# Performance work log

Hardware: AMD Instinct MI355X
Metric: run time of the kernel (lower is better)

Reference implementation:

```python
import jax, jax.numpy as jnp
import numpy as np

N_USER = 100000
N_ITEM = 100000
D = 64
N_INTER = 1600000
N_LAYERS = 3
REG_WEIGHT = 1e-4
BPR_GAMMA = 1e-10  # RecBole BPRLoss gamma
B, S = 4096, 6     # 1 positive + (S-2)=4 negatives per row


def setup_inputs() -> dict:
    rng = np.random.default_rng(0)
    u = rng.integers(0, N_USER, N_INTER)
    it = rng.integers(0, N_ITEM, N_INTER)
    pairs = np.unique(np.stack([u, it], 1), axis=0)  # dok dict dedupes
    u, it = pairs[:, 0], pairs[:, 1]
    N = N_USER + N_ITEM
    row = np.concatenate([u, it + N_USER])
    col = np.concatenate([it + N_USER, u])
    deg = np.bincount(row, minlength=N).astype(np.float64) + 1e-7
    dinv = np.power(deg, -0.5)
    val = (dinv[row] * dinv[col]).astype(np.float32)  # D^-1/2 A D^-1/2

    key = jax.random.key(0)
    k1, k2, k3, k4 = jax.random.split(key, 4)
    user_w = jax.random.normal(k1, (N_USER, D), jnp.float32) * 0.01
    item_w = jax.random.normal(k2, (N_ITEM, D), jnp.float32) * 0.01
    # padding_idx=0 -> row 0 zeroed
    user_w = user_w.at[0].set(0.0)
    item_w = item_w.at[0].set(0.0)

    xu = jax.random.randint(k3, (B, S, 1), 0, N_USER, jnp.int32)
    xi = jax.random.randint(k4, (B, S, 1), 0, N_ITEM, jnp.int32)
    pad = jnp.zeros((B, S, 2), jnp.int32)  # last 2 cols unused by forward
    x = jnp.concatenate([xu, xi, pad], axis=-1)

    return {
        "x": x,
        "user_w": user_w,
        "item_w": item_w,
        "adj_row": jnp.asarray(row, jnp.int32),
        "adj_col": jnp.asarray(col, jnp.int32),
        "adj_val": jnp.asarray(val, jnp.float32),
    }


def _propagate(user_w, item_w, adj_row, adj_col, adj_val):
    N = user_w.shape[0] + item_w.shape[0]
    h = jnp.concatenate([user_w, item_w], axis=0)  # [N, D]
    out = h  # layer-0 term of the stacked sum
    for i in range(N_LAYERS):
        # SpMM: h <- A_hat @ h  via gather + segment_sum over edges
        h = jax.ops.segment_sum(adj_val[:, None] * h[adj_col], adj_row, num_segments=N)
        # F.normalize(h, dim=-1)
        h = h / jnp.maximum(jnp.linalg.norm(h, axis=-1, keepdims=True), 1e-12)
        # result list appends h/(i+1) AND h each layer
        out = out + h / (i + 1) + h
    return out


def reference(x, user_w, item_w, adj_row, adj_col, adj_val):
    emb = _propagate(user_w, item_w, adj_row, adj_col, adj_val)
    user_emb, item_emb = emb[:N_USER], emb[N_USER:]

    p = x[:, 0, :]                       # [B, 4]
    n = x[:, 1:-1, :].reshape(-1, 4)     # [B*(S-2), 4]
    p_score = jnp.sum(user_emb[p[:, 0]] * item_emb[p[:, 1]], axis=-1)     # [B]
    n_score = jnp.sum(user_emb[n[:, 0]] * item_emb[n[:, 1]], axis=-1)
    n_score = n_score.reshape(x.shape[0], -1).sum(axis=-1)                # [B]

    bpr_loss = -jnp.mean(jnp.log(BPR_GAMMA + jax.nn.sigmoid(p_score - n_score)))
    # RecBole EmbLoss(norm=2): (||U||_F + ||I||_F) / n_item
    emb_loss = (jnp.linalg.norm(user_w) + jnp.linalg.norm(item_w)) / item_w.shape[0]
    return bpr_loss + REG_WEIGHT * emb_loss
```

## Files before the change

### kernel.cpp

```cpp
#include <hip/hip_runtime.h>
#include <hip/hip_fp16.h>

#define N_USER_C 100000
#define N_ITEM_C 100000
#define D_C 64
#define NN_C (N_USER_C + N_ITEM_C)
#define ND_C (NN_C * D_C)

#define BSHIFT 8
#define NBUCKET ((N_ITEM_C + 255) >> BSHIFT)
#define PB_CHUNK 8192

#define CONV_NBLK 1024
#define SCORE_NBLK 1024

typedef unsigned u32x4 __attribute__((ext_vector_type(4)));

union HP8 { u32x4 u; __half2 h[4]; };


__global__ __launch_bounds__(256) void edge_scan_kernel(
        const int* __restrict__ arow, const int* __restrict__ acol,
        int* __restrict__ bcnt, int* __restrict__ row_ptr_u, int ne) {
    __shared__ int s[NBUCKET];
    for (int i = threadIdx.x; i < NBUCKET; i += 256) s[i] = 0;
    __syncthreads();
    int stride = gridDim.x * blockDim.x;
    for (int e = blockIdx.x * blockDim.x + threadIdx.x; e <= ne; e += stride) {
        if (e < ne) atomicAdd(&s[(acol[e] - N_USER_C) >> BSHIFT], 1);
        int prev = (e == 0) ? -1 : arow[e - 1];
        int cur = (e == ne) ? N_USER_C : arow[e];
        for (int r = prev + 1; r <= cur; ++r) row_ptr_u[r] = e;
    }
    __syncthreads();
    for (int i = threadIdx.x; i < NBUCKET; i += 256)
        if (s[i]) atomicAdd(&bcnt[i], s[i]);
}

__global__ void bucket_scan_kernel(const int* __restrict__ bcnt, int* __restrict__ boff,
                                   int* __restrict__ row_ptr_i, int ne) {
    __shared__ int s[512];
    int t = threadIdx.x;
    s[t] = (t < NBUCKET) ? bcnt[t] : 0;
    __syncthreads();
    for (int o = 1; o < 512; o <<= 1) {
        int v = (t >= o) ? s[t - o] : 0;
        __syncthreads();
        s[t] += v;
        __syncthreads();
    }
    if (t < NBUCKET) boff[t] = (t == 0) ? 0 : s[t - 1];
    if (t == 0) { boff[NBUCKET] = ne; row_ptr_i[N_ITEM_C] = ne; }
}

__global__ __launch_bounds__(256) void bucket_scatter_kernel(
        const int* __restrict__ arow, const int* __restrict__ acol,
        const int* __restrict__ boff, int* __restrict__ bfill,
        int* __restrict__ staging, int ne) {
    __shared__ int hist[NBUCKET];
    __shared__ int base[NBUCKET];
    int nchunk = (ne + PB_CHUNK - 1) / PB_CHUNK;
    for (int ch = blockIdx.x; ch < nchunk; ch += gridDim.x) {
        int c0 = ch * PB_CHUNK;
        int c1 = c0 + PB_CHUNK; if (c1 > ne) c1 = ne;
        for (int i = threadIdx.x; i < NBUCKET; i += 256) hist[i] = 0;
        __syncthreads();
        for (int e = c0 + threadIdx.x; e < c1; e += 256)
            atomicAdd(&hist[(acol[e] - N_USER_C) >> BSHIFT], 1);
        __syncthreads();
        for (int i = threadIdx.x; i < NBUCKET; i += 256) {
            int h = hist[i];
            base[i] = h ? atomicAdd(&bfill[i], h) : 0;
            hist[i] = 0;
        }
        __syncthreads();
        for (int e = c0 + threadIdx.x; e < c1; e += 256) {
            int j = acol[e] - N_USER_C;
            int b = j >> BSHIFT;
            int p = atomicAdd(&hist[b], 1);
            staging[boff[b] + base[b] + p] = arow[e] | ((j & 255) << 24);
        }
        __syncthreads();
    }
}

__global__ __launch_bounds__(256) void bucket_finalize_kernel(
        const int* __restrict__ staging, const int* __restrict__ boff,
        int* __restrict__ row_ptr_i, int* __restrict__ csr_col) {
    __shared__ int cnt[256];
    __shared__ int incl[256];
    int b = blockIdx.x, t = threadIdx.x;
    int s0 = boff[b], s1 = boff[b + 1];
    cnt[t] = 0;
    __syncthreads();
    for (int e = s0 + t; e < s1; e += 256)
        atomicAdd(&cnt[((unsigned)staging[e]) >> 24], 1);
    __syncthreads();
    incl[t] = cnt[t];
    __syncthreads();
    for (int o = 1; o < 256; o <<= 1) {
        int v = (t >= o) ? incl[t - o] : 0;
        __syncthreads();
        incl[t] += v;
        __syncthreads();
    }
    int j = (b << BSHIFT) + t;
    if (j < N_ITEM_C) row_ptr_i[j] = s0 + ((t == 0) ? 0 : incl[t - 1]);
    cnt[t] = 0;
    __syncthreads();
    for (int e = s0 + t; e < s1; e += 256) {
        int w = staging[e];
        int jl = ((unsigned)w) >> 24;
        int p = atomicAdd(&cnt[jl], 1);
        int basej = (jl == 0) ? 0 : incl[jl - 1];
        csr_col[s0 + basej + p] = w & 0x00FFFFFF;
    }
}

__global__ void dinv_flag_kernel(const int* __restrict__ rpu, const int* __restrict__ rpi,
                                 const int* __restrict__ x,
                                 float* __restrict__ dinv, int* __restrict__ flags) {
    int r = blockIdx.x * blockDim.x + threadIdx.x;
    if (r < NN_C) {
        int deg = (r < N_USER_C) ? rpu[r + 1] - rpu[r]
                                 : rpi[r - N_USER_C + 1] - rpi[r - N_USER_C];
        double d = (double)deg + 1e-7;
        dinv[r] = (float)(1.0 / sqrt(d));
    }
    if (r < 4096 * 5) {
        int b = r / 5, s = r % 5;
        const int* xb = x + b * 24;
        flags[xb[s * 4]] = 1;
        flags[N_USER_C + xb[s * 4 + 1]] = 1;
    }
}

__global__ __launch_bounds__(256) void conv_ssq_kernel(
        const float4* __restrict__ uw, const float4* __restrict__ iw,
        const float* __restrict__ dinv, u32x4* __restrict__ wtab,
        float2* __restrict__ partial_sq) {
    __shared__ float s_u[4], s_i[4];
    int stride = gridDim.x * blockDim.x;
    int tot = ND_C / 8;
    int nu = N_USER_C * D_C / 8;
    float su = 0.f, si = 0.f;
    for (int i = blockIdx.x * blockDim.x + threadIdx.x; i < tot; i += stride) {
        bool user = i < nu;
        const float4* s = user ? (uw + (size_t)i * 2) : (iw + (size_t)(i - nu) * 2);
        float4 f0 = s[0], f1 = s[1];
        float d = f0.x * f0.x + f0.y * f0.y + f0.z * f0.z + f0.w * f0.w
                + f1.x * f1.x + f1.y * f1.y + f1.z * f1.z + f1.w * f1.w;
        if (user) su += d; else si += d;
        float dv = dinv[i >> 3];
        HP8 o;
        o.h[0] = __float22half2_rn(make_float2(dv * f0.x, dv * f0.y));
        o.h[1] = __float22half2_rn(make_float2(dv * f0.z, dv * f0.w));
        o.h[2] = __float22half2_rn(make_float2(dv * f1.x, dv * f1.y));
        o.h[3] = __float22half2_rn(make_float2(dv * f1.z, dv * f1.w));
        wtab[i] = o.u;
    }
    #pragma unroll
    for (int o = 1; o < 64; o <<= 1) { su += __shfl_xor(su, o); si += __shfl_xor(si, o); }
    int w = threadIdx.x >> 6;
    if ((threadIdx.x & 63) == 0) { s_u[w] = su; s_i[w] = si; }
    __syncthreads();
    if (threadIdx.x == 0)
        partial_sq[blockIdx.x] = make_float2(s_u[0] + s_u[1] + s_u[2] + s_u[3],
                                             s_i[0] + s_i[1] + s_i[2] + s_i[3]);
}


template <bool PRESCALE, bool SPARSE>
__global__ __launch_bounds__(256, 4) void spmv_kernel(
        const __half* __restrict__ hin, __half* __restrict__ hout,
        const int* __restrict__ row_ptr_u, const int* __restrict__ row_ptr_i,
        const int* __restrict__ acol, const int* __restrict__ csr_col,
        const int* __restrict__ flags, const float* __restrict__ dinv) {
    int gid = blockIdx.x * blockDim.x + threadIdx.x;
    int r = gid >> 3;
    int l = gid & 7;
    if (r >= NN_C) return;
    if (SPARSE && flags[r] == 0) return;

    int e0, e1;
    const int* __restrict__ cols;
    if (r < N_USER_C) { e0 = row_ptr_u[r]; e1 = row_ptr_u[r + 1]; cols = acol; }
    else {
        int rr = r - N_USER_C;
        e0 = row_ptr_i[rr]; e1 = row_ptr_i[rr + 1]; cols = csr_col;
    }

    auto srcH = [&](int c) -> const u32x4* {
        return reinterpret_cast<const u32x4*>(hin + (size_t)c * 64 + l * 8);
    };

    float a0[8] = {0}, a1[8] = {0};
    auto add8 = [&](float* a, const HP8& p) {
        #pragma unroll
        for (int k = 0; k < 4; ++k) {
            float2 f = __half22float2(p.h[k]);
            a[2 * k] += f.x; a[2 * k + 1] += f.y;
        }
    };

    int e = e0;
    for (; e + 4 <= e1; e += 4) {
        int c0 = cols[e], c1 = cols[e + 1], c2 = cols[e + 2], c3 = cols[e + 3];
        HP8 p0, p1, p2, p3;
        p0.u = *srcH(c0); p1.u = *srcH(c1); p2.u = *srcH(c2); p3.u = *srcH(c3);
        add8(a0, p0); add8(a1, p1); add8(a0, p2); add8(a1, p3);
    }
    for (; e < e1; ++e) {
        HP8 p0; p0.u = *srcH(cols[e]);
        add8(a0, p0);
    }

    float acc[8];
    float ss = 0.f;
    #pragma unroll
    for (int k = 0; k < 8; ++k) {
        acc[k] = a0[k] + a1[k];
        ss += acc[k] * acc[k];
    }
    ss += __shfl_xor(ss, 1);
    ss += __shfl_xor(ss, 2);
    ss += __shfl_xor(ss, 4);
    float scale = 1.0f / fmaxf(sqrtf(ss), 1e-12f);
    if (PRESCALE) scale *= dinv[r];

    HP8 o;
    #pragma unroll
    for (int k = 0; k < 4; ++k)
        o.h[k] = __float22half2_rn(make_float2(acc[2 * k] * scale, acc[2 * k + 1] * scale));
    *reinterpret_cast<u32x4*>(hout + (size_t)r * 64 + l * 8) = o.u;
}


__global__ void score_kernel(const int* __restrict__ x,
                             const float* __restrict__ uw, const float* __restrict__ iw,
                             const __half* __restrict__ h1, const __half* __restrict__ h2,
                             const __half* __restrict__ h3, const float* __restrict__ dinv,
                             float* __restrict__ partial_loss) {
    __shared__ float s_l[4];
    int wave = threadIdx.x >> 6;
    int lane = threadIdx.x & 63;
    int b = blockIdx.x * 4 + wave;
    const int* xb = x + b * 24;

    auto emb = [&](int r) -> float {
        size_t o = (size_t)r * 64 + lane;
        float base = (r < N_USER_C) ? uw[o] : iw[o - (size_t)N_USER_C * 64];
        float rs = 1.0f / dinv[r];
        return base + (2.0f * __half2float(h1[o]) + 1.5f * __half2float(h2[o])) * rs
                    + (4.0f / 3.0f) * __half2float(h3[o]);
    };

    float t = emb(xb[0]) * emb(N_USER_C + xb[1]);
    #pragma unroll
    for (int s = 1; s <= 4; ++s)
        t -= emb(xb[s * 4]) * emb(N_USER_C + xb[s * 4 + 1]);

    #pragma unroll
    for (int o = 1; o < 64; o <<= 1) t += __shfl_xor(t, o);
    if (lane == 0) {
        float sig = 1.0f / (1.0f + expf(-t));
        s_l[wave] = -logf(1e-10f + sig);
    }
    __syncthreads();
    if (threadIdx.x == 0)
        partial_loss[blockIdx.x] = s_l[0] + s_l[1] + s_l[2] + s_l[3];
}

__global__ void final_kernel(const float2* __restrict__ partial_sq,
                             const float* __restrict__ partial_loss,
                             float* __restrict__ out) {
    __shared__ float s_u[4], s_i[4], s_l[4];
    int t = threadIdx.x;
    int w = t >> 6, lane = t & 63;

    float su = 0.f, si = 0.f, lo = 0.f;
    #pragma unroll
    for (int k = 0; k < CONV_NBLK / 256; ++k) {
        float2 p = partial_sq[t + k * 256];
        su += p.x; si += p.y;
    }
    #pragma unroll
    for (int k = 0; k < SCORE_NBLK / 256; ++k) lo += partial_loss[t + k * 256];

    #pragma unroll
    for (int o = 1; o < 64; o <<= 1) {
        su += __shfl_xor(su, o);
        si += __shfl_xor(si, o);
        lo += __shfl_xor(lo, o);
    }
    if (lane == 0) { s_u[w] = su; s_i[w] = si; s_l[w] = lo; }
    __syncthreads();
    if (t == 0) {
        float tu = s_u[0] + s_u[1] + s_u[2] + s_u[3];
        float ti = s_i[0] + s_i[1] + s_i[2] + s_i[3];
        float tl = s_l[0] + s_l[1] + s_l[2] + s_l[3];
        float bpr = tl / 4096.0f;
        float emb_loss = (sqrtf(tu) + sqrtf(ti)) / (float)N_ITEM_C;
        out[0] = bpr + 1e-4f * emb_loss;
    }
}


extern "C" void kernel_launch(void* const* d_in, const int* in_sizes, int n_in,
                              void* d_out, int out_size, void* d_ws, size_t ws_size,
                              hipStream_t stream) {
    const int*   x    = (const int*)d_in[0];
    const float* uw   = (const float*)d_in[1];
    const float* iw   = (const float*)d_in[2];
    const int*   arow = (const int*)d_in[3];
    const int*   acol = (const int*)d_in[4];
    int nnz = in_sizes[3];
    int ne = nnz / 2;

    char* ws = (char*)d_ws;
    size_t off = 0;
    auto alloc = [&](size_t bytes) -> void* {
        void* p = ws + off;
        off += bytes;
        off = (off + 255) & ~(size_t)255;
        return p;
    };
    __half* wtab      = (__half*)alloc((size_t)ND_C * 2);
    __half* h1        = (__half*)alloc((size_t)ND_C * 2);
    __half* h2        = (__half*)alloc((size_t)ND_C * 2);
    __half* h3        = (__half*)alloc((size_t)ND_C * 2);
    int*    csr_col   = (int*)alloc((size_t)ne * 4);
    int*    row_ptr_u = (int*)alloc((size_t)(N_USER_C + 1) * 4);
    int*    row_ptr_i = (int*)alloc((size_t)(N_ITEM_C + 1) * 4);
    float*  dinv      = (float*)alloc((size_t)NN_C * 4);
    int*    flags     = (int*)alloc((size_t)NN_C * 4);
    int*    bmem      = (int*)alloc((size_t)2 * NBUCKET * 4);
    int*    boff      = (int*)alloc((size_t)(NBUCKET + 1) * 4);
    float2* psq       = (float2*)alloc((size_t)CONV_NBLK * 8);
    float*  ploss     = (float*)alloc((size_t)SCORE_NBLK * 4);
    int*    bcnt      = bmem;
    int*    bfill     = bmem + NBUCKET;
    int*    staging   = (int*)h3;

    hipMemsetAsync(bmem, 0, (size_t)2 * NBUCKET * 4, stream);
    hipMemsetAsync(flags, 0, (size_t)NN_C * 4, stream);

    edge_scan_kernel<<<256, 256, 0, stream>>>(arow, acol, bcnt, row_ptr_u, ne);
    bucket_scan_kernel<<<1, 512, 0, stream>>>(bcnt, boff, row_ptr_i, ne);
    int nchunk = (ne + PB_CHUNK - 1) / PB_CHUNK;
    bucket_scatter_kernel<<<nchunk, 256, 0, stream>>>(arow, acol, boff, bfill,
                                                      staging, ne);
    bucket_finalize_kernel<<<NBUCKET, 256, 0, stream>>>(staging, boff, row_ptr_i, csr_col);
    dinv_flag_kernel<<<(NN_C + 255) / 256, 256, 0, stream>>>(row_ptr_u, row_ptr_i,
                                                             x, dinv, flags);
    conv_ssq_kernel<<<CONV_NBLK, 256, 0, stream>>>((const float4*)uw, (const float4*)iw,
                                                   dinv, (u32x4*)wtab, psq);

    int grid = (NN_C * 8 + 255) / 256;
    spmv_kernel<true, false><<<grid, 256, 0, stream>>>(wtab, h1,
        row_ptr_u, row_ptr_i, acol, csr_col, flags, dinv);
    spmv_kernel<true, false><<<grid, 256, 0, stream>>>(h1, h2,
        row_ptr_u, row_ptr_i, acol, csr_col, flags, dinv);
    spmv_kernel<false, true><<<grid, 256, 0, stream>>>(h2, h3,
        row_ptr_u, row_ptr_i, acol, csr_col, flags, dinv);

    score_kernel<<<SCORE_NBLK, 256, 0, stream>>>(x, uw, iw, h1, h2, h3, dinv, ploss);
    final_kernel<<<1, 256, 0, stream>>>(psq, ploss, (float*)d_out);
}
```

Measured before the change: 340.5 us.

## Merge CSR build kernels, use fixed-capacity buckets and a compact third-layer worklist

Measured after the change: 318.8 us. 1.07x faster.

```diff
diff --git a/kernel.cpp b/kernel.cpp
--- a/kernel.cpp
+++ b/kernel.cpp
@@ -10,63 +10,39 @@
 #define BSHIFT 8
 #define NBUCKET ((N_ITEM_C + 255) >> BSHIFT)
 #define PB_CHUNK 8192
+#define BCAP 8192
 
 #define CONV_NBLK 1024
 #define SCORE_NBLK 1024
+#define NWORK_MAX (4096 * 5 * 2)
 
 typedef unsigned u32x4 __attribute__((ext_vector_type(4)));
 
 union HP8 { u32x4 u; __half2 h[4]; };
 
 
-__global__ __launch_bounds__(256) void edge_scan_kernel(
+__global__ __launch_bounds__(256) void scatter_kernel(
         const int* __restrict__ arow, const int* __restrict__ acol,
-        int* __restrict__ bcnt, int* __restrict__ row_ptr_u, int ne) {
-    __shared__ int s[NBUCKET];
-    for (int i = threadIdx.x; i < NBUCKET; i += 256) s[i] = 0;
-    __syncthreads();
-    int stride = gridDim.x * blockDim.x;
-    for (int e = blockIdx.x * blockDim.x + threadIdx.x; e <= ne; e += stride) {
-        if (e < ne) atomicAdd(&s[(acol[e] - N_USER_C) >> BSHIFT], 1);
-        int prev = (e == 0) ? -1 : arow[e - 1];
-        int cur = (e == ne) ? N_USER_C : arow[e];
-        for (int r = prev + 1; r <= cur; ++r) row_ptr_u[r] = e;
-    }
-    __syncthreads();
-    for (int i = threadIdx.x; i < NBUCKET; i += 256)
-        if (s[i]) atomicAdd(&bcnt[i], s[i]);
-}
-
-__global__ void bucket_scan_kernel(const int* __restrict__ bcnt, int* __restrict__ boff,
-                                   int* __restrict__ row_ptr_i, int ne) {
-    __shared__ int s[512];
-    int t = threadIdx.x;
-    s[t] = (t < NBUCKET) ? bcnt[t] : 0;
-    __syncthreads();
-    for (int o = 1; o < 512; o <<= 1) {
-        int v = (t >= o) ? s[t - o] : 0;
-        __syncthreads();
-        s[t] += v;
-        __syncthreads();
-    }
-    if (t < NBUCKET) boff[t] = (t == 0) ? 0 : s[t - 1];
-    if (t == 0) { boff[NBUCKET] = ne; row_ptr_i[N_ITEM_C] = ne; }
-}
-
-__global__ __launch_bounds__(256) void bucket_scatter_kernel(
-        const int* __restrict__ arow, const int* __restrict__ acol,
-        const int* __restrict__ boff, int* __restrict__ bfill,
-        int* __restrict__ staging, int ne) {
+        int* __restrict__ bfill, int* __restrict__ staging,
+        int* __restrict__ row_ptr_u, int ne) {
     __shared__ int hist[NBUCKET];
     __shared__ int base[NBUCKET];
+    if (blockIdx.x == 0 && threadIdx.x == 0) {
+        int last = arow[ne - 1];
+        for (int r = last + 1; r <= N_USER_C; ++r) row_ptr_u[r] = ne;
+    }
     int nchunk = (ne + PB_CHUNK - 1) / PB_CHUNK;
     for (int ch = blockIdx.x; ch < nchunk; ch += gridDim.x) {
         int c0 = ch * PB_CHUNK;
         int c1 = c0 + PB_CHUNK; if (c1 > ne) c1 = ne;
         for (int i = threadIdx.x; i < NBUCKET; i += 256) hist[i] = 0;
         __syncthreads();
-        for (int e = c0 + threadIdx.x; e < c1; e += 256)
+        for (int e = c0 + threadIdx.x; e < c1; e += 256) {
             atomicAdd(&hist[(acol[e] - N_USER_C) >> BSHIFT], 1);
+            int prev = (e == 0) ? -1 : arow[e - 1];
+            int cur = arow[e];
+            for (int r = prev + 1; r <= cur; ++r) row_ptr_u[r] = e;
+        }
         __syncthreads();
         for (int i = threadIdx.x; i < NBUCKET; i += 256) {
             int h = hist[i];
@@ -78,23 +54,24 @@
             int j = acol[e] - N_USER_C;
             int b = j >> BSHIFT;
             int p = atomicAdd(&hist[b], 1);
-            staging[boff[b] + base[b] + p] = arow[e] | ((j & 255) << 24);
+            staging[b * BCAP + base[b] + p] = arow[e] | ((j & 255) << 24);
         }
         __syncthreads();
     }
 }
 
-__global__ __launch_bounds__(256) void bucket_finalize_kernel(
-        const int* __restrict__ staging, const int* __restrict__ boff,
-        int* __restrict__ row_ptr_i, int* __restrict__ csr_col) {
+__global__ __launch_bounds__(256) void finalize_kernel(
+        const int* __restrict__ staging, const int* __restrict__ bfill,
+        int* __restrict__ rpi_packed, int* __restrict__ csr_col) {
     __shared__ int cnt[256];
     __shared__ int incl[256];
     int b = blockIdx.x, t = threadIdx.x;
-    int s0 = boff[b], s1 = boff[b + 1];
+    int n = bfill[b];
+    int s0 = b * BCAP;
     cnt[t] = 0;
     __syncthreads();
-    for (int e = s0 + t; e < s1; e += 256)
-        atomicAdd(&cnt[((unsigned)staging[e]) >> 24], 1);
+    for (int e = t; e < n; e += 256)
+        atomicAdd(&cnt[((unsigned)staging[s0 + e]) >> 24], 1);
     __syncthreads();
     incl[t] = cnt[t];
     __syncthreads();
@@ -104,12 +81,14 @@
         incl[t] += v;
         __syncthreads();
     }
+    int excl = (t == 0) ? 0 : incl[t - 1];
+    int mycnt = incl[t] - excl;
     int j = (b << BSHIFT) + t;
-    if (j < N_ITEM_C) row_ptr_i[j] = s0 + ((t == 0) ? 0 : incl[t - 1]);
+    if (j < N_ITEM_C) rpi_packed[j] = (s0 + excl) | (mycnt << 22);
     cnt[t] = 0;
     __syncthreads();
-    for (int e = s0 + t; e < s1; e += 256) {
-        int w = staging[e];
+    for (int e = t; e < n; e += 256) {
+        int w = staging[s0 + e];
         int jl = ((unsigned)w) >> 24;
         int p = atomicAdd(&cnt[jl], 1);
         int basej = (jl == 0) ? 0 : incl[jl - 1];
@@ -117,22 +96,34 @@
     }
 }
 
-__global__ void dinv_flag_kernel(const int* __restrict__ rpu, const int* __restrict__ rpi,
+__global__ void dinv_work_kernel(const int* __restrict__ rpu,
+                                 const int* __restrict__ rpi_packed,
                                  const int* __restrict__ x,
-                                 float* __restrict__ dinv, int* __restrict__ flags) {
-    int r = blockIdx.x * blockDim.x + threadIdx.x;
+                                 float* __restrict__ dinv,
+                                 int* __restrict__ wl, int* __restrict__ wl_cnt) {
+    __shared__ int lcnt, lbase;
+    int r = blockIdx.x * 256 + threadIdx.x;
     if (r < NN_C) {
         int deg = (r < N_USER_C) ? rpu[r + 1] - rpu[r]
-                                 : rpi[r - N_USER_C + 1] - rpi[r - N_USER_C];
+                                 : (int)(((unsigned)rpi_packed[r - N_USER_C]) >> 22);
         double d = (double)deg + 1e-7;
         dinv[r] = (float)(1.0 / sqrt(d));
     }
+    if (threadIdx.x == 0) lcnt = 0;
+    __syncthreads();
+    int rows[2]; int n = 0, loc = 0;
     if (r < 4096 * 5) {
         int b = r / 5, s = r % 5;
         const int* xb = x + b * 24;
-        flags[xb[s * 4]] = 1;
-        flags[N_USER_C + xb[s * 4 + 1]] = 1;
-    }
+        rows[0] = xb[s * 4];
+        rows[1] = N_USER_C + xb[s * 4 + 1];
+        n = 2;
+        loc = atomicAdd(&lcnt, 2);
+    }
+    __syncthreads();
+    if (threadIdx.x == 0) lbase = lcnt ? atomicAdd(wl_cnt, lcnt) : 0;
+    __syncthreads();
+    for (int i = 0; i < n; ++i) wl[lbase + loc + i] = rows[i];
 }
 
 __global__ __launch_bounds__(256) void conv_ssq_kernel(
@@ -170,24 +161,31 @@
 }
 
 
-template <bool PRESCALE, bool SPARSE>
+template <bool PRESCALE, bool WORK>
 __global__ __launch_bounds__(256, 4) void spmv_kernel(
         const __half* __restrict__ hin, __half* __restrict__ hout,
-        const int* __restrict__ row_ptr_u, const int* __restrict__ row_ptr_i,
+        const int* __restrict__ row_ptr_u, const int* __restrict__ rpi_packed,
         const int* __restrict__ acol, const int* __restrict__ csr_col,
-        const int* __restrict__ flags, const float* __restrict__ dinv) {
+        const int* __restrict__ wl, const int* __restrict__ wl_cnt,
+        const float* __restrict__ dinv) {
     int gid = blockIdx.x * blockDim.x + threadIdx.x;
-    int r = gid >> 3;
+    int slot = gid >> 3;
     int l = gid & 7;
-    if (r >= NN_C) return;
-    if (SPARSE && flags[r] == 0) return;
+    int r;
+    if (WORK) {
+        if (slot >= *wl_cnt) return;
+        r = wl[slot];
+    } else {
+        r = slot;
+        if (r >= NN_C) return;
+    }
 
     int e0, e1;
     const int* __restrict__ cols;
     if (r < N_USER_C) { e0 = row_ptr_u[r]; e1 = row_ptr_u[r + 1]; cols = acol; }
     else {
-        int rr = r - N_USER_C;
-        e0 = row_ptr_i[rr]; e1 = row_ptr_i[rr + 1]; cols = csr_col;
+        unsigned pk = (unsigned)rpi_packed[r - N_USER_C];
+        e0 = pk & 0x3FFFFF; e1 = e0 + (pk >> 22); cols = csr_col;
     }
 
     auto srcH = [&](int c) -> const u32x4* {
@@ -325,44 +323,41 @@
         off = (off + 255) & ~(size_t)255;
         return p;
     };
-    __half* wtab      = (__half*)alloc((size_t)ND_C * 2);
-    __half* h1        = (__half*)alloc((size_t)ND_C * 2);
-    __half* h2        = (__half*)alloc((size_t)ND_C * 2);
-    __half* h3        = (__half*)alloc((size_t)ND_C * 2);
-    int*    csr_col   = (int*)alloc((size_t)ne * 4);
-    int*    row_ptr_u = (int*)alloc((size_t)(N_USER_C + 1) * 4);
-    int*    row_ptr_i = (int*)alloc((size_t)(N_ITEM_C + 1) * 4);
-    float*  dinv      = (float*)alloc((size_t)NN_C * 4);
-    int*    flags     = (int*)alloc((size_t)NN_C * 4);
-    int*    bmem      = (int*)alloc((size_t)2 * NBUCKET * 4);
-    int*    boff      = (int*)alloc((size_t)(NBUCKET + 1) * 4);
-    float2* psq       = (float2*)alloc((size_t)CONV_NBLK * 8);
-    float*  ploss     = (float*)alloc((size_t)SCORE_NBLK * 4);
-    int*    bcnt      = bmem;
-    int*    bfill     = bmem + NBUCKET;
-    int*    staging   = (int*)h3;
-
-    hipMemsetAsync(bmem, 0, (size_t)2 * NBUCKET * 4, stream);
-    hipMemsetAsync(flags, 0, (size_t)NN_C * 4, stream);
-
-    edge_scan_kernel<<<256, 256, 0, stream>>>(arow, acol, bcnt, row_ptr_u, ne);
-    bucket_scan_kernel<<<1, 512, 0, stream>>>(bcnt, boff, row_ptr_i, ne);
+    __half* wtab       = (__half*)alloc((size_t)ND_C * 2);
+    __half* h1         = (__half*)alloc((size_t)ND_C * 2);
+    __half* h2         = (__half*)alloc((size_t)ND_C * 2);
+    __half* h3         = (__half*)alloc((size_t)ND_C * 2);
+    int*    csr_col    = (int*)alloc((size_t)NBUCKET * BCAP * 4);
+    int*    row_ptr_u  = (int*)alloc((size_t)(N_USER_C + 1) * 4);
+    int*    rpi_packed = (int*)alloc((size_t)N_ITEM_C * 4);
+    float*  dinv       = (float*)alloc((size_t)NN_C * 4);
+    int*    bmem       = (int*)alloc((size_t)(NBUCKET + 1) * 4);
+    int*    wl         = (int*)alloc((size_t)NWORK_MAX * 4);
+    float2* psq        = (float2*)alloc((size_t)CONV_NBLK * 8);
+    float*  ploss      = (float*)alloc((size_t)SCORE_NBLK * 4);
+    int*    bfill      = bmem;
+    int*    wl_cnt     = bmem + NBUCKET;
+    int*    staging    = (int*)h3;
+
+    hipMemsetAsync(bmem, 0, (size_t)(NBUCKET + 1) * 4, stream);
+
     int nchunk = (ne + PB_CHUNK - 1) / PB_CHUNK;
-    bucket_scatter_kernel<<<nchunk, 256, 0, stream>>>(arow, acol, boff, bfill,
-                                                      staging, ne);
-    bucket_finalize_kernel<<<NBUCKET, 256, 0, stream>>>(staging, boff, row_ptr_i, csr_col);
-    dinv_flag_kernel<<<(NN_C + 255) / 256, 256, 0, stream>>>(row_ptr_u, row_ptr_i,
-                                                             x, dinv, flags);
+    scatter_kernel<<<nchunk, 256, 0, stream>>>(arow, acol, bfill, staging,
+                                               row_ptr_u, ne);
+    finalize_kernel<<<NBUCKET, 256, 0, stream>>>(staging, bfill, rpi_packed, csr_col);
+    dinv_work_kernel<<<(NN_C + 255) / 256, 256, 0, stream>>>(row_ptr_u, rpi_packed,
+                                                             x, dinv, wl, wl_cnt);
     conv_ssq_kernel<<<CONV_NBLK, 256, 0, stream>>>((const float4*)uw, (const float4*)iw,
                                                    dinv, (u32x4*)wtab, psq);
 
     int grid = (NN_C * 8 + 255) / 256;
+    int wgrid = (NWORK_MAX * 8 + 255) / 256;
     spmv_kernel<true, false><<<grid, 256, 0, stream>>>(wtab, h1,
-        row_ptr_u, row_ptr_i, acol, csr_col, flags, dinv);
+        row_ptr_u, rpi_packed, acol, csr_col, wl, wl_cnt, dinv);
     spmv_kernel<true, false><<<grid, 256, 0, stream>>>(h1, h2,
-        row_ptr_u, row_ptr_i, acol, csr_col, flags, dinv);
-    spmv_kernel<false, true><<<grid, 256, 0, stream>>>(h2, h3,
-        row_ptr_u, row_ptr_i, acol, csr_col, flags, dinv);
+        row_ptr_u, rpi_packed, acol, csr_col, wl, wl_cnt, dinv);
+    spmv_kernel<false, true><<<wgrid, 256, 0, stream>>>(h2, h3,
+        row_ptr_u, rpi_packed, acol, csr_col, wl, wl_cnt, dinv);
 
     score_kernel<<<SCORE_NBLK, 256, 0, stream>>>(x, uw, iw, h1, h2, h3, dinv, ploss);
     final_kernel<<<1, 256, 0, stream>>>(psq, ploss, (float*)d_out);
```
